# Performance work log

Hardware: AMD Instinct MI355X
Metric: run time of the kernel (lower is better)

The kernel has to match this reference:

```python
import jax, jax.numpy as jnp
import numpy as np

N, F_DIM, H_DIM = 8192, 128, 128

def setup_inputs() -> dict:
    key = jax.random.key(0)
    ks = jax.random.split(key, 7)
    inp = {
        "input": jax.random.normal(ks[0], (N, F_DIM), dtype=jnp.float32),
        "wavelets": jax.random.normal(ks[1], (N, N), dtype=jnp.float32) / np.sqrt(N),
        "wavelets_inv": jax.random.normal(ks[2], (N, N), dtype=jnp.float32) / np.sqrt(N),
        # layer 1 params
        "W1": jax.random.uniform(ks[3], (F_DIM, H_DIM), dtype=jnp.float32,
                                 minval=-np.sqrt(6.0/(F_DIM+H_DIM)), maxval=np.sqrt(6.0/(F_DIM+H_DIM))),
        "f1": jax.random.uniform(ks[4], (N,), dtype=jnp.float32, minval=0.9, maxval=1.1),
        # layer 2 params
        "W2": jax.random.uniform(ks[5], (H_DIM, H_DIM), dtype=jnp.float32,
                                 minval=-np.sqrt(6.0/(H_DIM+H_DIM)), maxval=np.sqrt(6.0/(H_DIM+H_DIM))),
        "f2": jax.random.uniform(ks[6], (N,), dtype=jnp.float32, minval=0.9, maxval=1.1),
    }
    return inp

def _gwnn_layer(features, wavelets, wavelets_inv, W, filt):
    # torch: wavelets @ diag(filt) @ (wavelets_inv @ (features @ W))
    # diag(filt) matmul == column-wise scale of wavelets (broadcast elementwise)
    xw = features @ W                      # [N, out]
    spec = wavelets_inv @ xw               # [N, out] spectral-domain features
    spec = filt[:, None] * spec            # apply learnable diagonal filter
    return wavelets @ spec                 # [N, out]

def reference(input, wavelets, wavelets_inv, W1, f1, W2, f2):
    # eval mode: dropout is identity
    h1 = jax.nn.relu(_gwnn_layer(input, wavelets, wavelets_inv, W1, f1))
    out = _gwnn_layer(h1, wavelets, wavelets_inv, W2, f2)
    return out
```

## Files before the change

### kernel.cpp

```cpp
#include <hip/hip_runtime.h>
#include <hip/hip_bf16.h>
#include <stdint.h>


typedef __attribute__((ext_vector_type(4))) float f32x4;
typedef __attribute__((ext_vector_type(8))) short s16x8;
typedef __attribute__((ext_vector_type(4))) short s16x4;

#define DEVI static __device__ __forceinline__

DEVI short bf1(float x){ __bf16 h = (__bf16)x; return __builtin_bit_cast(short, h); }

DEVI s16x8 cvt8(f32x4 lo, f32x4 hi){
  s16x8 r;
#pragma unroll
  for (int i = 0; i < 4; ++i){ r[i] = bf1(lo[i]); r[4+i] = bf1(hi[i]); }
  return r;
}

DEVI void glds16(const void* g, void* l){
  __builtin_amdgcn_global_load_lds((const __attribute__((address_space(1))) void*)g,
                                   (__attribute__((address_space(3))) void*)l, 16, 0, 0);
}

template<int N> DEVI void waitvm(){
  if constexpr (N == 0)       asm volatile("s_waitcnt vmcnt(0)"  ::: "memory");
  else if constexpr (N == 5)  asm volatile("s_waitcnt vmcnt(5)"  ::: "memory");
  else if constexpr (N == 6)  asm volatile("s_waitcnt vmcnt(6)"  ::: "memory");
  else if constexpr (N == 10) asm volatile("s_waitcnt vmcnt(10)" ::: "memory");
}

__global__ __launch_bounds__(256, 1) void gemm_big(
    const float* __restrict__ Ap, const short* __restrict__ Btp,
    float* __restrict__ Pp, int K, int M)
{
  constexpr int BM = 256, BK = 32;
  constexpr int ASZ = BM*BK*4;
  constexpr int BSZ = 128*BK*2;
  constexpr int TSZ = ASZ + BSZ;
  constexpr int NBUF = 3, PRE = 2;
  __shared__ uint8_t lds[NBUF*TSZ];

  const int tid  = threadIdx.x;
  const int lane = tid & 63;
  const int wv   = tid >> 6;
  const int la   = lane & 15;
  const int g4   = lane >> 4;
  const int bxl  = ((blockIdx.x & 7) << 2) + (blockIdx.x >> 3);
  const int m0   = bxl * BM;
  const int kq   = blockIdx.y;
  const int K8   = K >> 3;
  const int kb   = kq * K8;

  const float* gAbase = Ap + (size_t)m0*K + kb;
  int aoffg[8];
#pragma unroll
  for (int j = 0; j < 8; ++j){
    const int rl = (wv<<6) + (j<<3) + (lane>>3);
    aoffg[j] = rl*K + (((lane&7) ^ (rl&7))<<2);
  }

  const int nb0 = (wv<<5) + (lane>>2);
  const short* gB0 = Btp + (size_t)(nb0    )*K + kb + (((lane&3)^(nb0&3))<<3);
  const short* gB1 = Btp + (size_t)(nb0+16 )*K + kb + (((lane&3)^(nb0&3))<<3);

  int aoff[4][2];
#pragma unroll
  for (int mi = 0; mi < 4; ++mi){
    const int r = (wv<<6) + mi*16 + la;
#pragma unroll
    for (int p = 0; p < 2; ++p)
      aoff[mi][p] = r*128 + ((((g4<<1)+p) ^ (r&7))<<4);
  }
  int boff[8];
#pragma unroll
  for (int ni = 0; ni < 8; ++ni){
    const int n = ni*16 + la;
    boff[ni] = n*64 + ((g4 ^ (n&3))<<4);
  }

  f32x4 acc[4][8] = {};

  int kk = 0;
  uint8_t* const lend = lds + NBUF*TSZ;
  uint8_t* bs = lds;
  uint8_t* bc = lds;

  auto STAGE = [&](){
    uint8_t* Ab = bs;
    uint8_t* Bb = bs + ASZ;
#pragma unroll
    for (int j = 0; j < 8; ++j)
      glds16(gAbase + aoffg[j] + kk, Ab + (wv<<13) + (j<<10));
    glds16(gB0, Bb + (wv<<11));
    glds16(gB1, Bb + (wv<<11) + 1024);
    gB0 += BK; gB1 += BK;
    kk += BK;
    bs += TSZ; if (bs == lend) bs = lds;
  };

  auto COMPUTE = [&](){
    const uint8_t* Ab = bc;
    const uint8_t* Bb = bc + ASZ;
    s16x8 a0 = cvt8(*(const f32x4*)(Ab + aoff[0][0]), *(const f32x4*)(Ab + aoff[0][1]));
    s16x8 a1 = cvt8(*(const f32x4*)(Ab + aoff[1][0]), *(const f32x4*)(Ab + aoff[1][1]));
    s16x8 a2 = cvt8(*(const f32x4*)(Ab + aoff[2][0]), *(const f32x4*)(Ab + aoff[2][1]));
    s16x8 a3 = cvt8(*(const f32x4*)(Ab + aoff[3][0]), *(const f32x4*)(Ab + aoff[3][1]));
#pragma unroll
    for (int ni = 0; ni < 8; ++ni){
      s16x8 b = *(const s16x8*)(Bb + boff[ni]);
      acc[0][ni] = __builtin_amdgcn_mfma_f32_16x16x32_bf16(a0, b, acc[0][ni], 0, 0, 0);
      acc[1][ni] = __builtin_amdgcn_mfma_f32_16x16x32_bf16(a1, b, acc[1][ni], 0, 0, 0);
      acc[2][ni] = __builtin_amdgcn_mfma_f32_16x16x32_bf16(a2, b, acc[2][ni], 0, 0, 0);
      acc[3][ni] = __builtin_amdgcn_mfma_f32_16x16x32_bf16(a3, b, acc[3][ni], 0, 0, 0);
    }
    bc += TSZ; if (bc == lend) bc = lds;
  };

  const int ns = K8 >> 5;
  for (int s = 0; s < PRE && s < ns; ++s) STAGE();

  for (int t = 0; t < ns; ++t){
    if (t < ns - 1) waitvm<10>();
    else            waitvm<0>();
    __builtin_amdgcn_s_barrier();
    asm volatile("" ::: "memory");
    if (t + PRE < ns) STAGE();
    COMPUTE();
    asm volatile("" ::: "memory");
  }

  float* P = Pp + (size_t)kq * M * 128;
  const int rbase = m0 + (wv<<6) + (g4<<2);
#pragma unroll
  for (int mi = 0; mi < 4; ++mi)
#pragma unroll
    for (int ni = 0; ni < 8; ++ni)
#pragma unroll
      for (int r = 0; r < 4; ++r)
        P[(size_t)(rbase + mi*16 + r)*128 + ni*16 + la] = acc[mi][ni][r];
}

template<bool ABF>
__global__ __launch_bounds__(256, 1) void sgemm(
    const void* __restrict__ Ap, const short* __restrict__ Btp,
    void* __restrict__ Outp, int K, int M)
{
  constexpr int BM = 32, BN = 128, BK = 64;
  constexpr int ASZ = ABF ? BM*BK*2 : BM*BK*4;
  constexpr int BSZ = BN*BK*2;
  constexpr int TSZ = ASZ + BSZ;
  constexpr int NL  = ABF ? 5 : 6;
  constexpr int NBUF = 3, PRE = 2;
  __shared__ uint8_t lds[NBUF*TSZ];

  const int tid  = threadIdx.x;
  const int lane = tid & 63;
  const int wv   = tid >> 6;
  const int la   = lane & 15;
  const int g4   = lane >> 4;
  const int m0   = blockIdx.x * BM;

  const float* gA0 = nullptr; const float* gA1 = nullptr; const short* gAh = nullptr;
  if constexpr (!ABF){
    const float* Af = (const float*)Ap;
    int r0 = (wv<<3) + (lane>>4);
    int r1 = r0 + 4;
    gA0 = Af + (size_t)(m0+r0)*K + (((lane&15)^(r0&15))<<2);
    gA1 = Af + (size_t)(m0+r1)*K + (((lane&15)^(r1&15))<<2);
  } else {
    const short* Ah = (const short*)Ap;
    int r = (wv<<3) + (lane>>3);
    gAh = Ah + (size_t)(m0+r)*K + (((lane&7)^(r&7))<<3);
  }
  const int nb0 = (wv<<5) + (lane>>3);
  const short* gB0 = Btp + (size_t)(nb0    )*K + (((lane&7)^(nb0&7))<<3);
  const short* gB1 = Btp + (size_t)(nb0+ 8 )*K + (((lane&7)^(nb0&7))<<3);
  const short* gB2 = Btp + (size_t)(nb0+16 )*K + (((lane&7)^(nb0&7))<<3);
  const short* gB3 = Btp + (size_t)(nb0+24 )*K + (((lane&7)^(nb0&7))<<3);

  int aoff[2][2][2];
  int boff[2][2];
#pragma unroll
  for (int mi = 0; mi < 2; ++mi){
    const int r = mi*16 + la;
#pragma unroll
    for (int kf = 0; kf < 2; ++kf){
      if constexpr (!ABF){
        const int v0 = kf*8 + (g4<<1);
        aoff[mi][kf][0] = r*256 + (((v0  )^(r&15))<<4);
        aoff[mi][kf][1] = r*256 + (((v0+1)^(r&15))<<4);
      } else {
        const int u = kf*4 + g4;
        aoff[mi][kf][0] = r*128 + ((u^(r&7))<<4);
        aoff[mi][kf][1] = 0;
      }
    }
  }
#pragma unroll
  for (int ni = 0; ni < 2; ++ni){
    const int n = (wv<<5) + ni*16 + la;
#pragma unroll
    for (int kf = 0; kf < 2; ++kf){
      const int u = kf*4 + g4;
      boff[ni][kf] = n*128 + ((u^(n&7))<<4);
    }
  }

  f32x4 acc[2][2] = {};

  auto STAGE = [&](uint8_t* buf){
    uint8_t* Ab = buf;
    uint8_t* Bb = buf + ASZ;
    if constexpr (!ABF){
      glds16(gA0, Ab + (wv<<11));
      glds16(gA1, Ab + (wv<<11) + 1024);
      gA0 += BK; gA1 += BK;
    } else {
      glds16(gAh, Ab + (wv<<10));
      gAh += BK;
    }
    glds16(gB0, Bb + (wv<<12));
    glds16(gB1, Bb + (wv<<12) + 1024);
    glds16(gB2, Bb + (wv<<12) + 2048);
    glds16(gB3, Bb + (wv<<12) + 3072);
    gB0 += BK; gB1 += BK; gB2 += BK; gB3 += BK;
  };

  auto COMPUTE = [&](const uint8_t* buf){
    const uint8_t* Ab = buf;
    const uint8_t* Bb = buf + ASZ;
#pragma unroll
    for (int kf = 0; kf < 2; ++kf){
      s16x8 a0, a1, b0, b1;
      if constexpr (!ABF){
        a0 = cvt8(*(const f32x4*)(Ab + aoff[0][kf][0]), *(const f32x4*)(Ab + aoff[0][kf][1]));
        a1 = cvt8(*(const f32x4*)(Ab + aoff[1][kf][0]), *(const f32x4*)(Ab + aoff[1][kf][1]));
      } else {
        a0 = *(const s16x8*)(Ab + aoff[0][kf][0]);
        a1 = *(const s16x8*)(Ab + aoff[1][kf][0]);
      }
      b0 = *(const s16x8*)(Bb + boff[0][kf]);
      b1 = *(const s16x8*)(Bb + boff[1][kf]);
      acc[0][0] = __builtin_amdgcn_mfma_f32_16x16x32_bf16(a0, b0, acc[0][0], 0, 0, 0);
      acc[0][1] = __builtin_amdgcn_mfma_f32_16x16x32_bf16(a0, b1, acc[0][1], 0, 0, 0);
      acc[1][0] = __builtin_amdgcn_mfma_f32_16x16x32_bf16(a1, b0, acc[1][0], 0, 0, 0);
      acc[1][1] = __builtin_amdgcn_mfma_f32_16x16x32_bf16(a1, b1, acc[1][1], 0, 0, 0);
    }
  };

  const int ns = K >> 6;
  uint8_t* const lend = lds + NBUF*TSZ;
  uint8_t* bs = lds;
  uint8_t* bc = lds;
  for (int s = 0; s < PRE && s < ns; ++s){
    STAGE(bs);
    bs += TSZ; if (bs == lend) bs = lds;
  }
  for (int t = 0; t < ns; ++t){
    if (t < ns - 1) waitvm<NL>(); else waitvm<0>();
    __builtin_amdgcn_s_barrier();
    asm volatile("" ::: "memory");
    if (t + PRE < ns){
      STAGE(bs);
      bs += TSZ; if (bs == lend) bs = lds;
    }
    COMPUTE(bc);
    bc += TSZ; if (bc == lend) bc = lds;
    asm volatile("" ::: "memory");
  }

  const int mbase = m0 + (g4<<2);
  const int nc0   = (wv<<5) + la;
#pragma unroll
  for (int mi = 0; mi < 2; ++mi){
#pragma unroll
    for (int ni = 0; ni < 2; ++ni){
      s16x4 pk;
#pragma unroll
      for (int r = 0; r < 4; ++r) pk[r] = bf1(acc[mi][ni][r]);
      *(s16x4*)((short*)Outp + (size_t)(nc0 + (ni<<4))*M + (mbase + (mi<<4))) = pk;
    }
  }
}


DEVI f32x4 sum8(const float* p, size_t S){
  f32x4 v = (*(const f32x4*)(p)       + *(const f32x4*)(p +   S))
          + (*(const f32x4*)(p + 2*S) + *(const f32x4*)(p + 3*S));
  f32x4 w = (*(const f32x4*)(p + 4*S) + *(const f32x4*)(p + 5*S))
          + (*(const f32x4*)(p + 6*S) + *(const f32x4*)(p + 7*S));
  return v + w;
}

__global__ __launch_bounds__(256) void red_t(
    const float* __restrict__ Pp, const float* __restrict__ fp,
    short* __restrict__ out, int M)
{
  __shared__ short t[128*65];
  const size_t S = (size_t)M*128;
  const int m0 = blockIdx.x * 64;
  const int tid = threadIdx.x;
#pragma unroll
  for (int it = 0; it < 8; ++it){
    const int idx = it*256 + tid;
    const int m = idx >> 5, nq = idx & 31;
    f32x4 v = sum8(Pp + (size_t)(m0+m)*128 + nq*4, S);
    const float fv = fp[m0+m];
#pragma unroll
    for (int j = 0; j < 4; ++j)
      t[(nq*4+j)*65 + m] = bf1(fv * v[j]);
  }
  __syncthreads();
#pragma unroll
  for (int it = 0; it < 8; ++it){
    const int idx = it*256 + tid;
    const int n = idx >> 4, mc = idx & 15;
    s16x4 v;
#pragma unroll
    for (int j = 0; j < 4; ++j) v[j] = t[n*65 + mc*4 + j];
    *(s16x4*)(out + (size_t)n*M + m0 + mc*4) = v;
  }
}

__global__ __launch_bounds__(256) void red_r(
    const float* __restrict__ Pp, short* __restrict__ out, int M)
{
  const size_t S = (size_t)M*128;
  const size_t i0 = (size_t)(blockIdx.x*256 + threadIdx.x) * 8;
  s16x8 v;
#pragma unroll
  for (int h = 0; h < 2; ++h){
    f32x4 a = sum8(Pp + i0 + 4*h, S);
#pragma unroll
    for (int j = 0; j < 4; ++j)
      v[4*h+j] = bf1(fmaxf(a[j], 0.0f));
  }
  *(s16x8*)(out + i0) = v;
}

__global__ __launch_bounds__(256) void red_f(
    const float* __restrict__ Pp, float* __restrict__ out, int M)
{
  const size_t S = (size_t)M*128;
  const size_t i0 = (size_t)(blockIdx.x*256 + threadIdx.x) * 4;
  *(f32x4*)(out + i0) = sum8(Pp + i0, S);
}

__global__ void wtrans_k(const float* __restrict__ W1, const float* __restrict__ W2,
                         short* __restrict__ T1, short* __restrict__ T2){
  const int idx = blockIdx.x*256 + threadIdx.x;
  const int m = idx >> 14, rem = idx & 16383;
  const int n = rem >> 7, k = rem & 127;
  const float* W = m ? W2 : W1;
  short* T = m ? T2 : T1;
  T[n*128 + k] = bf1(W[k*128 + n]);
}

extern "C" void kernel_launch(void* const* d_in, const int* in_sizes, int n_in,
                              void* d_out, int out_size, void* d_ws, size_t ws_size,
                              hipStream_t stream){
  const float* input = (const float*)d_in[0];
  const float* wav   = (const float*)d_in[1];
  const float* winv  = (const float*)d_in[2];
  const float* W1    = (const float*)d_in[3];
  const float* f1    = (const float*)d_in[4];
  const float* W2    = (const float*)d_in[5];
  const float* f2    = (const float*)d_in[6];

  constexpr int M = 8192;
  uint8_t* ws = (uint8_t*)d_ws;
  short* W1T = (short*)(ws);
  short* W2T = (short*)(ws + (32<<10));
  short* XWT = (short*)(ws + (64<<10));
  short* SPT = (short*)(ws + (64<<10) + (2<<20));
  short* H1  = (short*)(ws + (64<<10) + (4<<20));
  float* P   = (float*)(ws + (64<<10) + (6<<20));

  dim3 b(256);
  dim3 gbig(M/256, 8);
  dim3 gns(M/32);
  dim3 grt(M/64);
  dim3 grr(M*128/(256*8));
  dim3 grf(M*128/(256*4));
  dim3 gt(128);

  wtrans_k<<<gt, b, 0, stream>>>(W1, W2, W1T, W2T);
  sgemm<false><<<gns, b, 0, stream>>>(input, W1T, XWT, 128, M);
  gemm_big<<<gbig, b, 0, stream>>>(winv, XWT, P, M, M);
  red_t  <<<grt, b, 0, stream>>>(P, f1, SPT, M);
  gemm_big<<<gbig, b, 0, stream>>>(wav, SPT, P, M, M);
  red_r  <<<grr, b, 0, stream>>>(P, H1, M);
  sgemm<true ><<<gns, b, 0, stream>>>(H1, W2T, XWT, 128, M);
  gemm_big<<<gbig, b, 0, stream>>>(winv, XWT, P, M, M);
  red_t  <<<grt, b, 0, stream>>>(P, f2, SPT, M);
  gemm_big<<<gbig, b, 0, stream>>>(wav, SPT, P, M, M);
  red_f  <<<grf, b, 0, stream>>>(P, (float*)d_out, M);
}
```

Before: 339.5 us.

## Double K tile to 64 and switch gemm_big to double-buffered pipeline

Raises the K tile from 32 to 64 so each stage issues twice as many global-to-LDS loads and runs two MFMA k-fragments, and replaces the 3-buffer, prefetch-depth-2 ring with two buffers. Each iteration now issues the next stage's loads before waiting, then adds a second barrier after compute to protect buffer reuse. The aim is to halve loop iterations and barrier/wait overhead per unit of work. In exchange, the LDS footprint per buffer doubles, prefetch depth drops to one stage, and there is an extra barrier per iteration, which may expose more memory latency.

```diff
diff --git a/kernel.cpp b/kernel.cpp
--- a/kernel.cpp
+++ b/kernel.cpp
@@ -27,18 +27,18 @@
   if constexpr (N == 0)       asm volatile("s_waitcnt vmcnt(0)"  ::: "memory");
   else if constexpr (N == 5)  asm volatile("s_waitcnt vmcnt(5)"  ::: "memory");
   else if constexpr (N == 6)  asm volatile("s_waitcnt vmcnt(6)"  ::: "memory");
-  else if constexpr (N == 10) asm volatile("s_waitcnt vmcnt(10)" ::: "memory");
+  else if constexpr (N == 20) asm volatile("s_waitcnt vmcnt(20)" ::: "memory");
 }
 
 __global__ __launch_bounds__(256, 1) void gemm_big(
     const float* __restrict__ Ap, const short* __restrict__ Btp,
     float* __restrict__ Pp, int K, int M)
 {
-  constexpr int BM = 256, BK = 32;
+  constexpr int BM = 256, BK = 64;
   constexpr int ASZ = BM*BK*4;
   constexpr int BSZ = 128*BK*2;
   constexpr int TSZ = ASZ + BSZ;
-  constexpr int NBUF = 3, PRE = 2;
+  constexpr int NBUF = 2;
   __shared__ uint8_t lds[NBUF*TSZ];
 
   const int tid  = threadIdx.x;
@@ -53,36 +53,44 @@
   const int kb   = kq * K8;
 
   const float* gAbase = Ap + (size_t)m0*K + kb;
-  int aoffg[8];
-#pragma unroll
-  for (int j = 0; j < 8; ++j){
-    const int rl = (wv<<6) + (j<<3) + (lane>>3);
-    aoffg[j] = rl*K + (((lane&7) ^ (rl&7))<<2);
-  }
-
-  const int nb0 = (wv<<5) + (lane>>2);
-  const short* gB0 = Btp + (size_t)(nb0    )*K + kb + (((lane&3)^(nb0&3))<<3);
-  const short* gB1 = Btp + (size_t)(nb0+16 )*K + kb + (((lane&3)^(nb0&3))<<3);
-
-  int aoff[4][2];
+  int aoffg[16];
+#pragma unroll
+  for (int j = 0; j < 16; ++j){
+    const int rl = (wv<<6) + (j<<2) + (lane>>4);
+    aoffg[j] = rl*K + (((lane&15) ^ (rl&15))<<2);
+  }
+
+  const int nb0 = (wv<<5) + (lane>>3);
+  const short* gB0 = Btp + (size_t)(nb0    )*K + kb + (((lane&7)^(nb0&7))<<3);
+  const short* gB1 = Btp + (size_t)(nb0+ 8 )*K + kb + (((lane&7)^(nb0&7))<<3);
+  const short* gB2 = Btp + (size_t)(nb0+16 )*K + kb + (((lane&7)^(nb0&7))<<3);
+  const short* gB3 = Btp + (size_t)(nb0+24 )*K + kb + (((lane&7)^(nb0&7))<<3);
+
+  int aoff[4][2][2];
 #pragma unroll
   for (int mi = 0; mi < 4; ++mi){
     const int r = (wv<<6) + mi*16 + la;
 #pragma unroll
-    for (int p = 0; p < 2; ++p)
-      aoff[mi][p] = r*128 + ((((g4<<1)+p) ^ (r&7))<<4);
-  }
-  int boff[8];
+    for (int kf = 0; kf < 2; ++kf){
+      const int v0 = kf*8 + (g4<<1);
+      aoff[mi][kf][0] = r*256 + (((v0  )^(r&15))<<4);
+      aoff[mi][kf][1] = r*256 + (((v0+1)^(r&15))<<4);
+    }
+  }
+  int boff[8][2];
 #pragma unroll
   for (int ni = 0; ni < 8; ++ni){
     const int n = ni*16 + la;
-    boff[ni] = n*64 + ((g4 ^ (n&3))<<4);
+#pragma unroll
+    for (int kf = 0; kf < 2; ++kf){
+      const int u = kf*4 + g4;
+      boff[ni][kf] = n*128 + ((u^(n&7))<<4);
+    }
   }
 
   f32x4 acc[4][8] = {};
 
   int kk = 0;
-  uint8_t* const lend = lds + NBUF*TSZ;
   uint8_t* bs = lds;
   uint8_t* bc = lds;
 
@@ -90,44 +98,49 @@
     uint8_t* Ab = bs;
     uint8_t* Bb = bs + ASZ;
 #pragma unroll
-    for (int j = 0; j < 8; ++j)
-      glds16(gAbase + aoffg[j] + kk, Ab + (wv<<13) + (j<<10));
-    glds16(gB0, Bb + (wv<<11));
-    glds16(gB1, Bb + (wv<<11) + 1024);
-    gB0 += BK; gB1 += BK;
+    for (int j = 0; j < 16; ++j)
+      glds16(gAbase + aoffg[j] + kk, Ab + (wv<<14) + (j<<10));
     kk += BK;
-    bs += TSZ; if (bs == lend) bs = lds;
+    glds16(gB0, Bb + (wv<<12));
+    glds16(gB1, Bb + (wv<<12) + 1024);
+    glds16(gB2, Bb + (wv<<12) + 2048);
+    glds16(gB3, Bb + (wv<<12) + 3072);
+    gB0 += BK; gB1 += BK; gB2 += BK; gB3 += BK;
+    bs = (bs == lds) ? lds + TSZ : lds;
   };
 
   auto COMPUTE = [&](){
     const uint8_t* Ab = bc;
     const uint8_t* Bb = bc + ASZ;
-    s16x8 a0 = cvt8(*(const f32x4*)(Ab + aoff[0][0]), *(const f32x4*)(Ab + aoff[0][1]));
-    s16x8 a1 = cvt8(*(const f32x4*)(Ab + aoff[1][0]), *(const f32x4*)(Ab + aoff[1][1]));
-    s16x8 a2 = cvt8(*(const f32x4*)(Ab + aoff[2][0]), *(const f32x4*)(Ab + aoff[2][1]));
-    s16x8 a3 = cvt8(*(const f32x4*)(Ab + aoff[3][0]), *(const f32x4*)(Ab + aoff[3][1]));
-#pragma unroll
-    for (int ni = 0; ni < 8; ++ni){
-      s16x8 b = *(const s16x8*)(Bb + boff[ni]);
-      acc[0][ni] = __builtin_amdgcn_mfma_f32_16x16x32_bf16(a0, b, acc[0][ni], 0, 0, 0);
-      acc[1][ni] = __builtin_amdgcn_mfma_f32_16x16x32_bf16(a1, b, acc[1][ni], 0, 0, 0);
-      acc[2][ni] = __builtin_amdgcn_mfma_f32_16x16x32_bf16(a2, b, acc[2][ni], 0, 0, 0);
-      acc[3][ni] = __builtin_amdgcn_mfma_f32_16x16x32_bf16(a3, b, acc[3][ni], 0, 0, 0);
-    }
-    bc += TSZ; if (bc == lend) bc = lds;
+#pragma unroll
+    for (int kf = 0; kf < 2; ++kf){
+      s16x8 a0 = cvt8(*(const f32x4*)(Ab + aoff[0][kf][0]), *(const f32x4*)(Ab + aoff[0][kf][1]));
+      s16x8 a1 = cvt8(*(const f32x4*)(Ab + aoff[1][kf][0]), *(const f32x4*)(Ab + aoff[1][kf][1]));
+      s16x8 a2 = cvt8(*(const f32x4*)(Ab + aoff[2][kf][0]), *(const f32x4*)(Ab + aoff[2][kf][1]));
+      s16x8 a3 = cvt8(*(const f32x4*)(Ab + aoff[3][kf][0]), *(const f32x4*)(Ab + aoff[3][kf][1]));
+#pragma unroll
+      for (int ni = 0; ni < 8; ++ni){
+        s16x8 b = *(const s16x8*)(Bb + boff[ni][kf]);
+        acc[0][ni] = __builtin_amdgcn_mfma_f32_16x16x32_bf16(a0, b, acc[0][ni], 0, 0, 0);
+        acc[1][ni] = __builtin_amdgcn_mfma_f32_16x16x32_bf16(a1, b, acc[1][ni], 0, 0, 0);
+        acc[2][ni] = __builtin_amdgcn_mfma_f32_16x16x32_bf16(a2, b, acc[2][ni], 0, 0, 0);
+        acc[3][ni] = __builtin_amdgcn_mfma_f32_16x16x32_bf16(a3, b, acc[3][ni], 0, 0, 0);
+      }
+    }
+    bc = (bc == lds) ? lds + TSZ : lds;
   };
 
-  const int ns = K8 >> 5;
-  for (int s = 0; s < PRE && s < ns; ++s) STAGE();
+  const int ns = K8 >> 6;
+  STAGE();
 
   for (int t = 0; t < ns; ++t){
-    if (t < ns - 1) waitvm<10>();
-    else            waitvm<0>();
+    if (t + 1 < ns){ STAGE(); waitvm<20>(); }
+    else           { waitvm<0>(); }
     __builtin_amdgcn_s_barrier();
     asm volatile("" ::: "memory");
-    if (t + PRE < ns) STAGE();
     COMPUTE();
     asm volatile("" ::: "memory");
+    __builtin_amdgcn_s_barrier();
   }
 
   float* P = Pp + (size_t)kq * M * 128;
```

Result: faster. 325.7 us (-4.1%).
